# Kernel optimization log

Measured on AMD Instinct MI355X. Metric: run time of the kernel, lower is better.

The kernel has to match this reference:

```python
import jax, jax.numpy as jnp
import numpy as np

B, T, D = 128, 1024, 1024


def setup_inputs() -> dict:
    key = jax.random.key(0)
    ks = jax.random.split(key, 6)
    s = 0.02  # small init scale for weights
    return {
        "z_eeg": jax.random.normal(ks[0], (B, T, D), dtype=jnp.float32),
        "z_rppg": jax.random.normal(ks[1], (B, D), dtype=jnp.float32),
        "Wq": jax.random.normal(ks[2], (D, D), dtype=jnp.float32) * s,
        "Wk": jax.random.normal(ks[3], (D, D), dtype=jnp.float32) * s,
        "Wm_w": jax.random.normal(ks[4], (D, D), dtype=jnp.float32) * s,
        "Wm_b": jnp.zeros((D,), dtype=jnp.float32),
        "Wf_w": jax.random.normal(ks[5], (2 * D, D), dtype=jnp.float32) * s,
        "Wf_b": jnp.zeros((D,), dtype=jnp.float32),
        "bf": jnp.zeros((D,), dtype=jnp.float32),
    }


def reference(z_eeg, z_rppg, Wq, Wk, Wm_w, Wm_b, Wf_w, Wf_b, bf):
    d = Wq.shape[-1]
    Q = z_rppg @ Wq                                    # [B, D]
    K = jnp.einsum("btd,de->bte", z_eeg, Wk)          # [B, T, D]
    scores = jnp.einsum("bd,btd->bt", Q, K) / jnp.sqrt(jnp.float32(d))  # [B, T]
    w = jax.nn.softmax(scores, axis=1)                 # [B, T]
    A = jnp.einsum("bt,btd->bd", w, z_eeg)            # attention-pooled EEG [B, D]
    concat = jnp.concatenate([A, z_rppg], axis=-1)     # [B, 2D]
    f = jax.nn.sigmoid(concat @ Wf_w + Wf_b + bf)      # gate [B, D]
    m = A @ Wm_w + Wm_b                                # [B, D]
    h = jax.nn.relu(z_rppg + m * f)                    # gated residual fusion
    return h
```

## Files before the change

kernel.cpp:

```cpp
#include <hip/hip_runtime.h>
#include <hip/hip_bf16.h>


#define BB   128
#define TT   1024
#define DD   1024
#define NT   16
#define KS   32
#define QS   4

__global__ __launch_bounds__(256) void k_gemm_ab(const float* __restrict__ X,
                                                 const float* __restrict__ W,
                                                 float* __restrict__ Cpart) {
  const int t = threadIdx.x;
  const int ebase = blockIdx.x * 64;
  const int bbase = blockIdx.y * 16;
  const int p = blockIdx.z;
  const int e = ebase + (t & 63);
  const int bg = t >> 6;
  __shared__ __align__(16) float Xs[16][64];
  float acc[4] = {0.f, 0.f, 0.f, 0.f};
  const int kend = p * 256 + 256;
  for (int k0 = p * 256; k0 < kend; k0 += 64) {
#pragma unroll
    for (int j = 0; j < 4; ++j) {
      int i = t + 256 * j;
      Xs[i >> 6][i & 63] = X[(size_t)(bbase + (i >> 6)) * DD + k0 + (i & 63)];
    }
    __syncthreads();
#pragma unroll 16
    for (int kk = 0; kk < 64; ++kk) {
      float w = W[(size_t)(k0 + kk) * DD + e];
#pragma unroll
      for (int j = 0; j < 4; ++j) acc[j] = fmaf(Xs[bg + 4 * j][kk], w, acc[j]);
    }
    __syncthreads();
  }
#pragma unroll
  for (int j = 0; j < 4; ++j)
    Cpart[(size_t)p * BB * DD + (size_t)(bbase + bg + 4 * j) * DD + e] = acc[j];
}

__global__ __launch_bounds__(256) void k_gemm_abt(const float* __restrict__ Qpart,
                                                  const float* __restrict__ W,
                                                  float* __restrict__ Cpart) {
  const int t = threadIdx.x;
  const int dbase = blockIdx.x * 64;
  const int bbase = blockIdx.y * 16;
  const int p = blockIdx.z;
  const int dl = t & 63;
  const int bg = t >> 6;
  __shared__ __align__(16) float Xs[16][64];
  __shared__ __align__(16) float Ws[64][65];
  float acc[4] = {0.f, 0.f, 0.f, 0.f};
  const int kend = p * 256 + 256;
  for (int k0 = p * 256; k0 < kend; k0 += 64) {
#pragma unroll
    for (int j = 0; j < 4; ++j) {
      int i = t + 256 * j;
      const size_t base = (size_t)(bbase + (i >> 6)) * DD + k0 + (i & 63);
      float v = Qpart[base] + Qpart[base + (size_t)BB * DD] +
                Qpart[base + 2 * (size_t)BB * DD] + Qpart[base + 3 * (size_t)BB * DD];
      Xs[i >> 6][i & 63] = v;
    }
#pragma unroll
    for (int j = 0; j < 16; ++j) {
      int i = t + 256 * j;
      Ws[i >> 6][i & 63] = W[(size_t)(dbase + (i >> 6)) * DD + k0 + (i & 63)];
    }
    __syncthreads();
#pragma unroll 8
    for (int kk = 0; kk < 64; ++kk) {
      float w = Ws[dl][kk];
#pragma unroll
      for (int j = 0; j < 4; ++j) acc[j] = fmaf(Xs[bg + 4 * j][kk], w, acc[j]);
    }
    __syncthreads();
  }
#pragma unroll
  for (int j = 0; j < 4; ++j)
    Cpart[(size_t)p * BB * DD + (size_t)(bbase + bg + 4 * j) * DD + dbase + dl] = acc[j];
}

__global__ __launch_bounds__(256) void k_attn(const float* __restrict__ z_eeg,
                                              const float* __restrict__ Qkpart,
                                              float* __restrict__ Npart,
                                              float* __restrict__ Zpart) {
  const int t = threadIdx.x;
  const int lane = t & 63;
  const int w = t >> 6;
  const int tblk = blockIdx.x;
  const int b = blockIdx.y;

  float4 qk4[4];
#pragma unroll
  for (int q = 0; q < 4; ++q) {
    float4 a = ((const float4*)(Qkpart + (size_t)b * DD))[q * 64 + lane];
#pragma unroll
    for (int pp = 1; pp < QS; ++pp) {
      float4 s = ((const float4*)(Qkpart + ((size_t)pp * BB + b) * DD))[q * 64 + lane];
      a.x += s.x; a.y += s.y; a.z += s.z; a.w += s.w;
    }
    a.x *= 0.03125f; a.y *= 0.03125f; a.z *= 0.03125f; a.w *= 0.03125f;
    qk4[q] = a;
  }

  float4 acc[4] = {};
  float zsum = 0.f;
  const float4* zb = (const float4*)(z_eeg + (size_t)b * TT * DD);
  const int row0 = tblk * 64 + w;

  float4 cA[4], cB[4];
  {
    const float4* pA = zb + (size_t)row0 * 256;
    const float4* pB = zb + (size_t)(row0 + 4) * 256;
#pragma unroll
    for (int q = 0; q < 4; ++q) cA[q] = pA[q * 64 + lane];
#pragma unroll
    for (int q = 0; q < 4; ++q) cB[q] = pB[q * 64 + lane];
  }
#pragma unroll
  for (int i = 0; i < 8; ++i) {
    float4 nA[4], nB[4];
    if (i < 7) {
      const float4* pA = zb + (size_t)(row0 + (i + 1) * 8) * 256;
      const float4* pB = zb + (size_t)(row0 + (i + 1) * 8 + 4) * 256;
#pragma unroll
      for (int q = 0; q < 4; ++q) nA[q] = pA[q * 64 + lane];
#pragma unroll
      for (int q = 0; q < 4; ++q) nB[q] = pB[q * 64 + lane];
    }
    float dotA = 0.f, dotB = 0.f;
#pragma unroll
    for (int q = 0; q < 4; ++q) {
      dotA += cA[q].x * qk4[q].x + cA[q].y * qk4[q].y + cA[q].z * qk4[q].z + cA[q].w * qk4[q].w;
      dotB += cB[q].x * qk4[q].x + cB[q].y * qk4[q].y + cB[q].z * qk4[q].z + cB[q].w * qk4[q].w;
    }
#pragma unroll
    for (int off = 32; off >= 1; off >>= 1) {
      dotA += __shfl_xor(dotA, off);
      dotB += __shfl_xor(dotB, off);
    }
    const float eA = __expf(dotA);
    const float eB = __expf(dotB);
    zsum += eA + eB;
#pragma unroll
    for (int q = 0; q < 4; ++q) {
      acc[q].x = fmaf(eA, cA[q].x, acc[q].x);
      acc[q].y = fmaf(eA, cA[q].y, acc[q].y);
      acc[q].z = fmaf(eA, cA[q].z, acc[q].z);
      acc[q].w = fmaf(eA, cA[q].w, acc[q].w);
      acc[q].x = fmaf(eB, cB[q].x, acc[q].x);
      acc[q].y = fmaf(eB, cB[q].y, acc[q].y);
      acc[q].z = fmaf(eB, cB[q].z, acc[q].z);
      acc[q].w = fmaf(eB, cB[q].w, acc[q].w);
    }
    if (i < 7) {
#pragma unroll
      for (int q = 0; q < 4; ++q) { cA[q] = nA[q]; cB[q] = nB[q]; }
    }
  }

  __shared__ __align__(16) float4 sacc[3][256];
  __shared__ float szw[4];
  if (w > 0) {
#pragma unroll
    for (int q = 0; q < 4; ++q) sacc[w - 1][q * 64 + lane] = acc[q];
  }
  if (lane == 0) szw[w] = zsum;
  __syncthreads();
  if (w == 0) {
    float4* np = (float4*)(Npart + ((size_t)b * NT + tblk) * DD);
#pragma unroll
    for (int q = 0; q < 4; ++q) {
      float4 a = acc[q];
#pragma unroll
      for (int ww = 0; ww < 3; ++ww) {
        float4 s = sacc[ww][q * 64 + lane];
        a.x += s.x; a.y += s.y; a.z += s.z; a.w += s.w;
      }
      np[q * 64 + lane] = a;
    }
    if (lane == 0) Zpart[b * NT + tblk] = szw[0] + szw[1] + szw[2] + szw[3];
  }
}

__global__ __launch_bounds__(256) void k_reduce_a(const float* __restrict__ Npart,
                                                  const float* __restrict__ Zpart,
                                                  float* __restrict__ A) {
  const int idx = blockIdx.x * 256 + threadIdx.x;
  const int b = idx >> 10;
  const int d = idx & 1023;
  float n = 0.f, z = 0.f;
#pragma unroll
  for (int k = 0; k < NT; ++k) {
    n += Npart[((size_t)b * NT + k) * DD + d];
    z += Zpart[b * NT + k];
  }
  A[idx] = n / z;
}

__device__ __forceinline__ void outer_acc(float4 acc[4], const float4 a, const float4 w) {
  acc[0].x = fmaf(a.x, w.x, acc[0].x); acc[0].y = fmaf(a.x, w.y, acc[0].y);
  acc[0].z = fmaf(a.x, w.z, acc[0].z); acc[0].w = fmaf(a.x, w.w, acc[0].w);
  acc[1].x = fmaf(a.y, w.x, acc[1].x); acc[1].y = fmaf(a.y, w.y, acc[1].y);
  acc[1].z = fmaf(a.y, w.z, acc[1].z); acc[1].w = fmaf(a.y, w.w, acc[1].w);
  acc[2].x = fmaf(a.z, w.x, acc[2].x); acc[2].y = fmaf(a.z, w.y, acc[2].y);
  acc[2].z = fmaf(a.z, w.z, acc[2].z); acc[2].w = fmaf(a.z, w.w, acc[2].w);
  acc[3].x = fmaf(a.w, w.x, acc[3].x); acc[3].y = fmaf(a.w, w.y, acc[3].y);
  acc[3].z = fmaf(a.w, w.z, acc[3].z); acc[3].w = fmaf(a.w, w.w, acc[3].w);
}

__global__ __launch_bounds__(256) void k_epi_partial(const float* __restrict__ A,
                                                     const float* __restrict__ z_rppg,
                                                     const float* __restrict__ Wf_w,
                                                     const float* __restrict__ Wm_w,
                                                     float* __restrict__ fpart,
                                                     float* __restrict__ mpart) {
  const int t = threadIdx.x;
  const int dbase = blockIdx.x * 32;
  const int ks = blockIdx.y;
  const int bq = t >> 3;
  const int dg = t & 7;
  __shared__ __align__(16) float Cst[32][132];
  __shared__ __align__(16) float Ws[32][36];
  float4 accf[4] = {};
  float4 accm[4] = {};

  {
    const float* src = (ks < 16) ? (A + ks * 64) : (z_rppg + ks * 64 - 1024);
    const float* wsrc = Wf_w + (size_t)ks * 64 * DD;
    for (int k0 = 0; k0 < 64; k0 += 32) {
#pragma unroll
      for (int j = 0; j < 16; ++j) {
        int i = t + 256 * j; int bb = i >> 5, c = i & 31;
        Cst[c][bb] = src[(size_t)bb * DD + k0 + c];
      }
#pragma unroll
      for (int j = 0; j < 4; ++j) {
        int i = t + 256 * j; int r = i >> 5, c = i & 31;
        Ws[r][c] = wsrc[(size_t)(k0 + r) * DD + dbase + c];
      }
      __syncthreads();
#pragma unroll
      for (int kk = 0; kk < 32; ++kk) {
        float4 a4 = *(const float4*)&Cst[kk][bq * 4];
        float4 w4 = *(const float4*)&Ws[kk][dg * 4];
        outer_acc(accf, a4, w4);
      }
      __syncthreads();
    }
  }
  {
    const float* src = A + ks * 32;
    const float* wsrc = Wm_w + (size_t)ks * 32 * DD;
#pragma unroll
    for (int j = 0; j < 16; ++j) {
      int i = t + 256 * j; int bb = i >> 5, c = i & 31;
      Cst[c][bb] = src[(size_t)bb * DD + c];
    }
#pragma unroll
    for (int j = 0; j < 4; ++j) {
      int i = t + 256 * j; int r = i >> 5, c = i & 31;
      Ws[r][c] = wsrc[(size_t)r * DD + dbase + c];
    }
    __syncthreads();
#pragma unroll
    for (int kk = 0; kk < 32; ++kk) {
      float4 a4 = *(const float4*)&Cst[kk][bq * 4];
      float4 w4 = *(const float4*)&Ws[kk][dg * 4];
      outer_acc(accm, a4, w4);
    }
  }
#pragma unroll
  for (int i = 0; i < 4; ++i) {
    const int b = bq * 4 + i;
    *(float4*)&fpart[(size_t)ks * (BB * DD) + (size_t)b * DD + dbase + dg * 4] = accf[i];
    *(float4*)&mpart[(size_t)ks * (BB * DD) + (size_t)b * DD + dbase + dg * 4] = accm[i];
  }
}

__global__ __launch_bounds__(256) void k_combine(const float* __restrict__ fpart,
                                                 const float* __restrict__ mpart,
                                                 const float* __restrict__ Wf_b,
                                                 const float* __restrict__ bf,
                                                 const float* __restrict__ Wm_b,
                                                 const float* __restrict__ z_rppg,
                                                 float* __restrict__ out) {
  const int idx = blockIdx.x * 256 + threadIdx.x;
  const int d = idx & 1023;
  float f = Wf_b[d] + bf[d];
  float m = Wm_b[d];
#pragma unroll
  for (int k = 0; k < KS; ++k) {
    f += fpart[(size_t)k * (BB * DD) + idx];
    m += mpart[(size_t)k * (BB * DD) + idx];
  }
  const float g = 1.f / (1.f + __expf(-f));
  const float h = z_rppg[idx] + m * g;
  out[idx] = h > 0.f ? h : 0.f;
}

extern "C" void kernel_launch(void* const* d_in, const int* in_sizes, int n_in,
                              void* d_out, int out_size, void* d_ws, size_t ws_size,
                              hipStream_t stream) {
  const float* z_eeg  = (const float*)d_in[0];
  const float* z_rppg = (const float*)d_in[1];
  const float* Wq     = (const float*)d_in[2];
  const float* Wk     = (const float*)d_in[3];
  const float* Wm_w   = (const float*)d_in[4];
  const float* Wm_b   = (const float*)d_in[5];
  const float* Wf_w   = (const float*)d_in[6];
  const float* Wf_b   = (const float*)d_in[7];
  const float* bf     = (const float*)d_in[8];
  float* out = (float*)d_out;

  float* ws = (float*)d_ws;
  float* Qpart  = ws;
  float* Qkpart = Qpart + (size_t)QS * BB * DD;
  float* Npart  = Qkpart + (size_t)QS * BB * DD;
  float* Zpart  = Npart + (size_t)BB * NT * DD;
  float* A      = Zpart + BB * NT;
  float* fpart  = A + (size_t)BB * DD;
  float* mpart  = fpart + (size_t)KS * BB * DD;

  k_gemm_ab<<<dim3(16, 8, QS), 256, 0, stream>>>(z_rppg, Wq, Qpart);
  k_gemm_abt<<<dim3(16, 8, QS), 256, 0, stream>>>(Qpart, Wk, Qkpart);
  k_attn<<<dim3(NT, BB), 256, 0, stream>>>(z_eeg, Qkpart, Npart, Zpart);
  k_reduce_a<<<(BB * DD) / 256, 256, 0, stream>>>(Npart, Zpart, A);
  k_epi_partial<<<dim3(32, KS), 256, 0, stream>>>(A, z_rppg, Wf_w, Wm_w, fpart, mpart);
  k_combine<<<(BB * DD) / 256, 256, 0, stream>>>(fpart, mpart, Wf_b, bf, Wm_b, z_rppg, out);
}
```

Before: 225.9 us.

## Fuse all stages into one persistent kernel with software grid barriers

Replaces six separate kernel launches with a single persistent kernel of 256 blocks that runs the Q GEMM, Wk projection, attention pooling, normalization, gate/mix GEMMs and combine in sequence. Stages are separated by atomic-counter grid barriers. Work partitioning changes: attention uses two blocks per batch row, and the epilogue uses 16 K-splits instead of 32. This aims to remove launch gaps and shrink partial-sum buffers. The tradeoffs are low occupancy during the bandwidth-heavy attention pass and a reliance on all blocks being co-resident.

Measured after the change: 260.1 us. +15.2%, slower.

```diff
diff --git a/kernel.cpp b/kernel.cpp
--- a/kernel.cpp
+++ b/kernel.cpp
@@ -5,199 +5,32 @@
 #define BB   128
 #define TT   1024
 #define DD   1024
-#define NT   16
-#define KS   32
+#define NB   256
+#define NTH  512
 #define QS   4
-
-__global__ __launch_bounds__(256) void k_gemm_ab(const float* __restrict__ X,
-                                                 const float* __restrict__ W,
-                                                 float* __restrict__ Cpart) {
-  const int t = threadIdx.x;
-  const int ebase = blockIdx.x * 64;
-  const int bbase = blockIdx.y * 16;
-  const int p = blockIdx.z;
-  const int e = ebase + (t & 63);
-  const int bg = t >> 6;
-  __shared__ __align__(16) float Xs[16][64];
-  float acc[4] = {0.f, 0.f, 0.f, 0.f};
-  const int kend = p * 256 + 256;
-  for (int k0 = p * 256; k0 < kend; k0 += 64) {
-#pragma unroll
-    for (int j = 0; j < 4; ++j) {
-      int i = t + 256 * j;
-      Xs[i >> 6][i & 63] = X[(size_t)(bbase + (i >> 6)) * DD + k0 + (i & 63)];
-    }
-    __syncthreads();
-#pragma unroll 16
-    for (int kk = 0; kk < 64; ++kk) {
-      float w = W[(size_t)(k0 + kk) * DD + e];
-#pragma unroll
-      for (int j = 0; j < 4; ++j) acc[j] = fmaf(Xs[bg + 4 * j][kk], w, acc[j]);
-    }
-    __syncthreads();
-  }
-#pragma unroll
-  for (int j = 0; j < 4; ++j)
-    Cpart[(size_t)p * BB * DD + (size_t)(bbase + bg + 4 * j) * DD + e] = acc[j];
-}
-
-__global__ __launch_bounds__(256) void k_gemm_abt(const float* __restrict__ Qpart,
-                                                  const float* __restrict__ W,
-                                                  float* __restrict__ Cpart) {
-  const int t = threadIdx.x;
-  const int dbase = blockIdx.x * 64;
-  const int bbase = blockIdx.y * 16;
-  const int p = blockIdx.z;
-  const int dl = t & 63;
-  const int bg = t >> 6;
-  __shared__ __align__(16) float Xs[16][64];
-  __shared__ __align__(16) float Ws[64][65];
-  float acc[4] = {0.f, 0.f, 0.f, 0.f};
-  const int kend = p * 256 + 256;
-  for (int k0 = p * 256; k0 < kend; k0 += 64) {
-#pragma unroll
-    for (int j = 0; j < 4; ++j) {
-      int i = t + 256 * j;
-      const size_t base = (size_t)(bbase + (i >> 6)) * DD + k0 + (i & 63);
-      float v = Qpart[base] + Qpart[base + (size_t)BB * DD] +
-                Qpart[base + 2 * (size_t)BB * DD] + Qpart[base + 3 * (size_t)BB * DD];
-      Xs[i >> 6][i & 63] = v;
-    }
-#pragma unroll
-    for (int j = 0; j < 16; ++j) {
-      int i = t + 256 * j;
-      Ws[i >> 6][i & 63] = W[(size_t)(dbase + (i >> 6)) * DD + k0 + (i & 63)];
-    }
-    __syncthreads();
-#pragma unroll 8
-    for (int kk = 0; kk < 64; ++kk) {
-      float w = Ws[dl][kk];
-#pragma unroll
-      for (int j = 0; j < 4; ++j) acc[j] = fmaf(Xs[bg + 4 * j][kk], w, acc[j]);
-    }
-    __syncthreads();
-  }
-#pragma unroll
-  for (int j = 0; j < 4; ++j)
-    Cpart[(size_t)p * BB * DD + (size_t)(bbase + bg + 4 * j) * DD + dbase + dl] = acc[j];
-}
-
-__global__ __launch_bounds__(256) void k_attn(const float* __restrict__ z_eeg,
-                                              const float* __restrict__ Qkpart,
-                                              float* __restrict__ Npart,
-                                              float* __restrict__ Zpart) {
-  const int t = threadIdx.x;
-  const int lane = t & 63;
-  const int w = t >> 6;
-  const int tblk = blockIdx.x;
-  const int b = blockIdx.y;
-
-  float4 qk4[4];
-#pragma unroll
-  for (int q = 0; q < 4; ++q) {
-    float4 a = ((const float4*)(Qkpart + (size_t)b * DD))[q * 64 + lane];
-#pragma unroll
-    for (int pp = 1; pp < QS; ++pp) {
-      float4 s = ((const float4*)(Qkpart + ((size_t)pp * BB + b) * DD))[q * 64 + lane];
-      a.x += s.x; a.y += s.y; a.z += s.z; a.w += s.w;
-    }
-    a.x *= 0.03125f; a.y *= 0.03125f; a.z *= 0.03125f; a.w *= 0.03125f;
-    qk4[q] = a;
-  }
-
-  float4 acc[4] = {};
-  float zsum = 0.f;
-  const float4* zb = (const float4*)(z_eeg + (size_t)b * TT * DD);
-  const int row0 = tblk * 64 + w;
-
-  float4 cA[4], cB[4];
-  {
-    const float4* pA = zb + (size_t)row0 * 256;
-    const float4* pB = zb + (size_t)(row0 + 4) * 256;
-#pragma unroll
-    for (int q = 0; q < 4; ++q) cA[q] = pA[q * 64 + lane];
-#pragma unroll
-    for (int q = 0; q < 4; ++q) cB[q] = pB[q * 64 + lane];
-  }
-#pragma unroll
-  for (int i = 0; i < 8; ++i) {
-    float4 nA[4], nB[4];
-    if (i < 7) {
-      const float4* pA = zb + (size_t)(row0 + (i + 1) * 8) * 256;
-      const float4* pB = zb + (size_t)(row0 + (i + 1) * 8 + 4) * 256;
-#pragma unroll
-      for (int q = 0; q < 4; ++q) nA[q] = pA[q * 64 + lane];
-#pragma unroll
-      for (int q = 0; q < 4; ++q) nB[q] = pB[q * 64 + lane];
-    }
-    float dotA = 0.f, dotB = 0.f;
-#pragma unroll
-    for (int q = 0; q < 4; ++q) {
-      dotA += cA[q].x * qk4[q].x + cA[q].y * qk4[q].y + cA[q].z * qk4[q].z + cA[q].w * qk4[q].w;
-      dotB += cB[q].x * qk4[q].x + cB[q].y * qk4[q].y + cB[q].z * qk4[q].z + cB[q].w * qk4[q].w;
-    }
-#pragma unroll
-    for (int off = 32; off >= 1; off >>= 1) {
-      dotA += __shfl_xor(dotA, off);
-      dotB += __shfl_xor(dotB, off);
-    }
-    const float eA = __expf(dotA);
-    const float eB = __expf(dotB);
-    zsum += eA + eB;
-#pragma unroll
-    for (int q = 0; q < 4; ++q) {
-      acc[q].x = fmaf(eA, cA[q].x, acc[q].x);
-      acc[q].y = fmaf(eA, cA[q].y, acc[q].y);
-      acc[q].z = fmaf(eA, cA[q].z, acc[q].z);
-      acc[q].w = fmaf(eA, cA[q].w, acc[q].w);
-      acc[q].x = fmaf(eB, cB[q].x, acc[q].x);
-      acc[q].y = fmaf(eB, cB[q].y, acc[q].y);
-      acc[q].z = fmaf(eB, cB[q].z, acc[q].z);
-      acc[q].w = fmaf(eB, cB[q].w, acc[q].w);
-    }
-    if (i < 7) {
-#pragma unroll
-      for (int q = 0; q < 4; ++q) { cA[q] = nA[q]; cB[q] = nB[q]; }
-    }
-  }
-
-  __shared__ __align__(16) float4 sacc[3][256];
-  __shared__ float szw[4];
-  if (w > 0) {
-#pragma unroll
-    for (int q = 0; q < 4; ++q) sacc[w - 1][q * 64 + lane] = acc[q];
-  }
-  if (lane == 0) szw[w] = zsum;
+#define KSE  16
+
+union SharedU {
+  struct { float Xs[16][64]; float Ws[128][65]; } g;
+  struct { float4 sacc[8][256]; float szw[8]; } a;
+  struct { float Cst[32][132]; float Wst[32][68]; } e;
+};
+
+__device__ __forceinline__ void gsync(int* cnt, int* rel, int gen) {
   __syncthreads();
-  if (w == 0) {
-    float4* np = (float4*)(Npart + ((size_t)b * NT + tblk) * DD);
-#pragma unroll
-    for (int q = 0; q < 4; ++q) {
-      float4 a = acc[q];
-#pragma unroll
-      for (int ww = 0; ww < 3; ++ww) {
-        float4 s = sacc[ww][q * 64 + lane];
-        a.x += s.x; a.y += s.y; a.z += s.z; a.w += s.w;
-      }
-      np[q * 64 + lane] = a;
-    }
-    if (lane == 0) Zpart[b * NT + tblk] = szw[0] + szw[1] + szw[2] + szw[3];
-  }
-}
-
-__global__ __launch_bounds__(256) void k_reduce_a(const float* __restrict__ Npart,
-                                                  const float* __restrict__ Zpart,
-                                                  float* __restrict__ A) {
-  const int idx = blockIdx.x * 256 + threadIdx.x;
-  const int b = idx >> 10;
-  const int d = idx & 1023;
-  float n = 0.f, z = 0.f;
-#pragma unroll
-  for (int k = 0; k < NT; ++k) {
-    n += Npart[((size_t)b * NT + k) * DD + d];
-    z += Zpart[b * NT + k];
-  }
-  A[idx] = n / z;
+  if (threadIdx.x == 0) {
+    __threadfence();
+    int old = __hip_atomic_fetch_add(cnt, 1, __ATOMIC_RELAXED, __HIP_MEMORY_SCOPE_AGENT);
+    if (old == NB * gen - 1) {
+      __hip_atomic_store(rel, gen, __ATOMIC_RELAXED, __HIP_MEMORY_SCOPE_AGENT);
+    } else {
+      while (__hip_atomic_load(rel, __ATOMIC_RELAXED, __HIP_MEMORY_SCOPE_AGENT) < gen) {
+        __builtin_amdgcn_s_sleep(2);
+      }
+    }
+    __threadfence();
+  }
+  __syncthreads();
 }
 
 __device__ __forceinline__ void outer_acc(float4 acc[4], const float4 a, const float4 w) {
@@ -211,94 +44,268 @@
   acc[3].z = fmaf(a.w, w.z, acc[3].z); acc[3].w = fmaf(a.w, w.w, acc[3].w);
 }
 
-__global__ __launch_bounds__(256) void k_epi_partial(const float* __restrict__ A,
-                                                     const float* __restrict__ z_rppg,
-                                                     const float* __restrict__ Wf_w,
-                                                     const float* __restrict__ Wm_w,
-                                                     float* __restrict__ fpart,
-                                                     float* __restrict__ mpart) {
+__global__ __launch_bounds__(NTH, 2) void k_fused(
+    const float* __restrict__ z_eeg, const float* __restrict__ z_rppg,
+    const float* __restrict__ Wq, const float* __restrict__ Wk,
+    const float* __restrict__ Wm_w, const float* __restrict__ Wm_b,
+    const float* __restrict__ Wf_w, const float* __restrict__ Wf_b,
+    const float* __restrict__ bfp, float* __restrict__ out,
+    float* __restrict__ Qpart, float* __restrict__ Qkpart,
+    float* __restrict__ Npart, float* __restrict__ Zpart,
+    float* __restrict__ A, float* __restrict__ fpart, float* __restrict__ mpart,
+    int* cnt, int* rel) {
+  __shared__ SharedU sh;
   const int t = threadIdx.x;
-  const int dbase = blockIdx.x * 32;
-  const int ks = blockIdx.y;
-  const int bq = t >> 3;
-  const int dg = t & 7;
-  __shared__ __align__(16) float Cst[32][132];
-  __shared__ __align__(16) float Ws[32][36];
-  float4 accf[4] = {};
-  float4 accm[4] = {};
-
-  {
-    const float* src = (ks < 16) ? (A + ks * 64) : (z_rppg + ks * 64 - 1024);
-    const float* wsrc = Wf_w + (size_t)ks * 64 * DD;
-    for (int k0 = 0; k0 < 64; k0 += 32) {
+  const int bid = blockIdx.x;
+
+  {
+    const int ebase = (bid & 7) * 128;
+    const int bbase = ((bid >> 3) & 7) * 16;
+    const int p = bid >> 6;
+    const int e = ebase + (t & 127);
+    const int bg = t >> 7;
+    float acc[4] = {0.f, 0.f, 0.f, 0.f};
+    const int kend = p * 256 + 256;
+    for (int k0 = p * 256; k0 < kend; k0 += 64) {
+#pragma unroll
+      for (int j = 0; j < 2; ++j) {
+        int i = t + NTH * j;
+        sh.g.Xs[i >> 6][i & 63] = z_rppg[(size_t)(bbase + (i >> 6)) * DD + k0 + (i & 63)];
+      }
+      __syncthreads();
+#pragma unroll 16
+      for (int kk = 0; kk < 64; ++kk) {
+        float w = Wq[(size_t)(k0 + kk) * DD + e];
+#pragma unroll
+        for (int j = 0; j < 4; ++j) acc[j] = fmaf(sh.g.Xs[bg + 4 * j][kk], w, acc[j]);
+      }
+      __syncthreads();
+    }
+#pragma unroll
+    for (int j = 0; j < 4; ++j)
+      Qpart[(size_t)p * BB * DD + (size_t)(bbase + bg + 4 * j) * DD + e] = acc[j];
+  }
+  gsync(cnt, rel, 1);
+
+  {
+    const int dbase = (bid & 7) * 128;
+    const int bbase = ((bid >> 3) & 7) * 16;
+    const int p = bid >> 6;
+    const int dl = t & 127;
+    const int bg = t >> 7;
+    float acc[4] = {0.f, 0.f, 0.f, 0.f};
+    const int kend = p * 256 + 256;
+    for (int k0 = p * 256; k0 < kend; k0 += 64) {
+#pragma unroll
+      for (int j = 0; j < 2; ++j) {
+        int i = t + NTH * j;
+        const size_t base = (size_t)(bbase + (i >> 6)) * DD + k0 + (i & 63);
+        sh.g.Xs[i >> 6][i & 63] = Qpart[base] + Qpart[base + (size_t)BB * DD] +
+                                  Qpart[base + 2 * (size_t)BB * DD] +
+                                  Qpart[base + 3 * (size_t)BB * DD];
+      }
 #pragma unroll
       for (int j = 0; j < 16; ++j) {
-        int i = t + 256 * j; int bb = i >> 5, c = i & 31;
-        Cst[c][bb] = src[(size_t)bb * DD + k0 + c];
-      }
-#pragma unroll
-      for (int j = 0; j < 4; ++j) {
-        int i = t + 256 * j; int r = i >> 5, c = i & 31;
-        Ws[r][c] = wsrc[(size_t)(k0 + r) * DD + dbase + c];
+        int i = t + NTH * j;
+        sh.g.Ws[i >> 6][i & 63] = Wk[(size_t)(dbase + (i >> 6)) * DD + k0 + (i & 63)];
       }
       __syncthreads();
-#pragma unroll
-      for (int kk = 0; kk < 32; ++kk) {
-        float4 a4 = *(const float4*)&Cst[kk][bq * 4];
-        float4 w4 = *(const float4*)&Ws[kk][dg * 4];
-        outer_acc(accf, a4, w4);
+#pragma unroll 8
+      for (int kk = 0; kk < 64; ++kk) {
+        float w = sh.g.Ws[dl][kk];
+#pragma unroll
+        for (int j = 0; j < 4; ++j) acc[j] = fmaf(sh.g.Xs[bg + 4 * j][kk], w, acc[j]);
       }
       __syncthreads();
     }
-  }
-  {
-    const float* src = A + ks * 32;
-    const float* wsrc = Wm_w + (size_t)ks * 32 * DD;
-#pragma unroll
-    for (int j = 0; j < 16; ++j) {
-      int i = t + 256 * j; int bb = i >> 5, c = i & 31;
-      Cst[c][bb] = src[(size_t)bb * DD + c];
-    }
-#pragma unroll
-    for (int j = 0; j < 4; ++j) {
-      int i = t + 256 * j; int r = i >> 5, c = i & 31;
-      Ws[r][c] = wsrc[(size_t)r * DD + dbase + c];
-    }
+#pragma unroll
+    for (int j = 0; j < 4; ++j)
+      Qkpart[(size_t)p * BB * DD + (size_t)(bbase + bg + 4 * j) * DD + dbase + dl] = acc[j];
+  }
+  gsync(cnt, rel, 2);
+
+  {
+    const int b = bid >> 1;
+    const int th = bid & 1;
+    const int lane = t & 63;
+    const int w = t >> 6;
+
+    float4 qk4[4];
+#pragma unroll
+    for (int q = 0; q < 4; ++q) {
+      float4 a = ((const float4*)(Qkpart + (size_t)b * DD))[q * 64 + lane];
+#pragma unroll
+      for (int pp = 1; pp < QS; ++pp) {
+        float4 s = ((const float4*)(Qkpart + ((size_t)pp * BB + b) * DD))[q * 64 + lane];
+        a.x += s.x; a.y += s.y; a.z += s.z; a.w += s.w;
+      }
+      a.x *= 0.03125f; a.y *= 0.03125f; a.z *= 0.03125f; a.w *= 0.03125f;
+      qk4[q] = a;
+    }
+
+    float4 acc[4] = {};
+    float zsum = 0.f;
+    const float4* zb = (const float4*)(z_eeg + (size_t)b * TT * DD);
+    const int rbase = th * 512 + w * 4;
+
+    for (int i = 0; i < 16; ++i) {
+      const int r0 = rbase + i * 32;
+      const float4* p0 = zb + (size_t)(r0 + 0) * 256;
+      const float4* p1 = zb + (size_t)(r0 + 1) * 256;
+      const float4* p2 = zb + (size_t)(r0 + 2) * 256;
+      const float4* p3 = zb + (size_t)(r0 + 3) * 256;
+      float4 z0[4], z1[4], z2[4], z3[4];
+#pragma unroll
+      for (int q = 0; q < 4; ++q) z0[q] = p0[q * 64 + lane];
+#pragma unroll
+      for (int q = 0; q < 4; ++q) z1[q] = p1[q * 64 + lane];
+#pragma unroll
+      for (int q = 0; q < 4; ++q) z2[q] = p2[q * 64 + lane];
+#pragma unroll
+      for (int q = 0; q < 4; ++q) z3[q] = p3[q * 64 + lane];
+      float d0 = 0.f, d1 = 0.f, d2 = 0.f, d3 = 0.f;
+#pragma unroll
+      for (int q = 0; q < 4; ++q) {
+        d0 += z0[q].x * qk4[q].x + z0[q].y * qk4[q].y + z0[q].z * qk4[q].z + z0[q].w * qk4[q].w;
+        d1 += z1[q].x * qk4[q].x + z1[q].y * qk4[q].y + z1[q].z * qk4[q].z + z1[q].w * qk4[q].w;
+        d2 += z2[q].x * qk4[q].x + z2[q].y * qk4[q].y + z2[q].z * qk4[q].z + z2[q].w * qk4[q].w;
+        d3 += z3[q].x * qk4[q].x + z3[q].y * qk4[q].y + z3[q].z * qk4[q].z + z3[q].w * qk4[q].w;
+      }
+#pragma unroll
+      for (int off = 32; off >= 1; off >>= 1) {
+        d0 += __shfl_xor(d0, off);
+        d1 += __shfl_xor(d1, off);
+        d2 += __shfl_xor(d2, off);
+        d3 += __shfl_xor(d3, off);
+      }
+      const float e0 = __expf(d0);
+      const float e1 = __expf(d1);
+      const float e2 = __expf(d2);
+      const float e3 = __expf(d3);
+      zsum += e0 + e1 + e2 + e3;
+#pragma unroll
+      for (int q = 0; q < 4; ++q) {
+        acc[q].x = fmaf(e0, z0[q].x, acc[q].x); acc[q].y = fmaf(e0, z0[q].y, acc[q].y);
+        acc[q].z = fmaf(e0, z0[q].z, acc[q].z); acc[q].w = fmaf(e0, z0[q].w, acc[q].w);
+        acc[q].x = fmaf(e1, z1[q].x, acc[q].x); acc[q].y = fmaf(e1, z1[q].y, acc[q].y);
+        acc[q].z = fmaf(e1, z1[q].z, acc[q].z); acc[q].w = fmaf(e1, z1[q].w, acc[q].w);
+        acc[q].x = fmaf(e2, z2[q].x, acc[q].x); acc[q].y = fmaf(e2, z2[q].y, acc[q].y);
+        acc[q].z = fmaf(e2, z2[q].z, acc[q].z); acc[q].w = fmaf(e2, z2[q].w, acc[q].w);
+        acc[q].x = fmaf(e3, z3[q].x, acc[q].x); acc[q].y = fmaf(e3, z3[q].y, acc[q].y);
+        acc[q].z = fmaf(e3, z3[q].z, acc[q].z); acc[q].w = fmaf(e3, z3[q].w, acc[q].w);
+      }
+    }
+
+#pragma unroll
+    for (int q = 0; q < 4; ++q) sh.a.sacc[w][q * 64 + lane] = acc[q];
+    if (lane == 0) sh.a.szw[w] = zsum;
     __syncthreads();
-#pragma unroll
-    for (int kk = 0; kk < 32; ++kk) {
-      float4 a4 = *(const float4*)&Cst[kk][bq * 4];
-      float4 w4 = *(const float4*)&Ws[kk][dg * 4];
-      outer_acc(accm, a4, w4);
-    }
-  }
-#pragma unroll
-  for (int i = 0; i < 4; ++i) {
-    const int b = bq * 4 + i;
-    *(float4*)&fpart[(size_t)ks * (BB * DD) + (size_t)b * DD + dbase + dg * 4] = accf[i];
-    *(float4*)&mpart[(size_t)ks * (BB * DD) + (size_t)b * DD + dbase + dg * 4] = accm[i];
-  }
-}
-
-__global__ __launch_bounds__(256) void k_combine(const float* __restrict__ fpart,
-                                                 const float* __restrict__ mpart,
-                                                 const float* __restrict__ Wf_b,
-                                                 const float* __restrict__ bf,
-                                                 const float* __restrict__ Wm_b,
-                                                 const float* __restrict__ z_rppg,
-                                                 float* __restrict__ out) {
-  const int idx = blockIdx.x * 256 + threadIdx.x;
-  const int d = idx & 1023;
-  float f = Wf_b[d] + bf[d];
-  float m = Wm_b[d];
-#pragma unroll
-  for (int k = 0; k < KS; ++k) {
-    f += fpart[(size_t)k * (BB * DD) + idx];
-    m += mpart[(size_t)k * (BB * DD) + idx];
-  }
-  const float g = 1.f / (1.f + __expf(-f));
-  const float h = z_rppg[idx] + m * g;
-  out[idx] = h > 0.f ? h : 0.f;
+    if (t < 256) {
+      float4 s = sh.a.sacc[0][t];
+#pragma unroll
+      for (int ww = 1; ww < 8; ++ww) {
+        float4 v = sh.a.sacc[ww][t];
+        s.x += v.x; s.y += v.y; s.z += v.z; s.w += v.w;
+      }
+      ((float4*)(Npart + (size_t)bid * DD))[t] = s;
+      if (t == 0) {
+        float z = 0.f;
+#pragma unroll
+        for (int ww = 0; ww < 8; ++ww) z += sh.a.szw[ww];
+        Zpart[bid] = z;
+      }
+    }
+  }
+  gsync(cnt, rel, 3);
+
+  {
+    const int idx = bid * NTH + t;
+    const int b = idx >> 10;
+    const int d = idx & 1023;
+    float n = Npart[(size_t)(2 * b) * DD + d] + Npart[(size_t)(2 * b + 1) * DD + d];
+    float z = Zpart[2 * b] + Zpart[2 * b + 1];
+    A[idx] = n / z;
+  }
+  gsync(cnt, rel, 4);
+
+  {
+    const int dbase = (bid & 15) * 64;
+    const int ks = bid >> 4;
+    const int bq = t >> 4;
+    const int dg = t & 15;
+    float4 accf[4] = {};
+    float4 accm[4] = {};
+    {
+      const float* src = (ks < 8) ? (A + ks * 128) : (z_rppg + (ks - 8) * 128);
+      const float* wsrc = Wf_w + (size_t)ks * 128 * DD;
+      for (int k0 = 0; k0 < 128; k0 += 32) {
+#pragma unroll
+        for (int j = 0; j < 8; ++j) {
+          int i = t + NTH * j; int bb = i >> 5, c = i & 31;
+          sh.e.Cst[c][bb] = src[(size_t)bb * DD + k0 + c];
+        }
+#pragma unroll
+        for (int j = 0; j < 4; ++j) {
+          int i = t + NTH * j; int r = i >> 6, c = i & 63;
+          sh.e.Wst[r][c] = wsrc[(size_t)(k0 + r) * DD + dbase + c];
+        }
+        __syncthreads();
+#pragma unroll
+        for (int kk = 0; kk < 32; ++kk) {
+          float4 a4 = *(const float4*)&sh.e.Cst[kk][bq * 4];
+          float4 w4 = *(const float4*)&sh.e.Wst[kk][dg * 4];
+          outer_acc(accf, a4, w4);
+        }
+        __syncthreads();
+      }
+    }
+    {
+      const float* src = A + ks * 64;
+      const float* wsrc = Wm_w + (size_t)ks * 64 * DD;
+      for (int k0 = 0; k0 < 64; k0 += 32) {
+#pragma unroll
+        for (int j = 0; j < 8; ++j) {
+          int i = t + NTH * j; int bb = i >> 5, c = i & 31;
+          sh.e.Cst[c][bb] = src[(size_t)bb * DD + k0 + c];
+        }
+#pragma unroll
+        for (int j = 0; j < 4; ++j) {
+          int i = t + NTH * j; int r = i >> 6, c = i & 63;
+          sh.e.Wst[r][c] = wsrc[(size_t)(k0 + r) * DD + dbase + c];
+        }
+        __syncthreads();
+#pragma unroll
+        for (int kk = 0; kk < 32; ++kk) {
+          float4 a4 = *(const float4*)&sh.e.Cst[kk][bq * 4];
+          float4 w4 = *(const float4*)&sh.e.Wst[kk][dg * 4];
+          outer_acc(accm, a4, w4);
+        }
+        __syncthreads();
+      }
+    }
+#pragma unroll
+    for (int i = 0; i < 4; ++i) {
+      const int b = bq * 4 + i;
+      *(float4*)&fpart[(size_t)ks * (BB * DD) + (size_t)b * DD + dbase + dg * 4] = accf[i];
+      *(float4*)&mpart[(size_t)ks * (BB * DD) + (size_t)b * DD + dbase + dg * 4] = accm[i];
+    }
+  }
+  gsync(cnt, rel, 5);
+
+  {
+    const int idx = bid * NTH + t;
+    const int d = idx & 1023;
+    float f = Wf_b[d] + bfp[d];
+    float m = Wm_b[d];
+#pragma unroll
+    for (int k = 0; k < KSE; ++k) {
+      f += fpart[(size_t)k * (BB * DD) + idx];
+      m += mpart[(size_t)k * (BB * DD) + idx];
+    }
+    const float g = 1.f / (1.f + __expf(-f));
+    const float h = z_rppg[idx] + m * g;
+    out[idx] = h > 0.f ? h : 0.f;
+  }
 }
 
 extern "C" void kernel_launch(void* const* d_in, const int* in_sizes, int n_in,
@@ -312,22 +319,23 @@
   const float* Wm_b   = (const float*)d_in[5];
   const float* Wf_w   = (const float*)d_in[6];
   const float* Wf_b   = (const float*)d_in[7];
-  const float* bf     = (const float*)d_in[8];
+  const float* bfp    = (const float*)d_in[8];
   float* out = (float*)d_out;
 
-  float* ws = (float*)d_ws;
-  float* Qpart  = ws;
+  int* cnt = (int*)d_ws;
+  int* rel = cnt + 1;
+  hipMemsetAsync(d_ws, 0, 16, stream);
+
+  float* base   = (float*)d_ws + 256;
+  float* Qpart  = base;
   float* Qkpart = Qpart + (size_t)QS * BB * DD;
   float* Npart  = Qkpart + (size_t)QS * BB * DD;
-  float* Zpart  = Npart + (size_t)BB * NT * DD;
-  float* A      = Zpart + BB * NT;
+  float* Zpart  = Npart + (size_t)2 * BB * DD;
+  float* A      = Zpart + 2 * BB;
   float* fpart  = A + (size_t)BB * DD;
-  float* mpart  = fpart + (size_t)KS * BB * DD;
-
-  k_gemm_ab<<<dim3(16, 8, QS), 256, 0, stream>>>(z_rppg, Wq, Qpart);
-  k_gemm_abt<<<dim3(16, 8, QS), 256, 0, stream>>>(Qpart, Wk, Qkpart);
-  k_attn<<<dim3(NT, BB), 256, 0, stream>>>(z_eeg, Qkpart, Npart, Zpart);
-  k_reduce_a<<<(BB * DD) / 256, 256, 0, stream>>>(Npart, Zpart, A);
-  k_epi_partial<<<dim3(32, KS), 256, 0, stream>>>(A, z_rppg, Wf_w, Wm_w, fpart, mpart);
-  k_combine<<<(BB * DD) / 256, 256, 0, stream>>>(fpart, mpart, Wf_b, bf, Wm_b, z_rppg, out);
+  float* mpart  = fpart + (size_t)KSE * BB * DD;
+
+  k_fused<<<NB, NTH, 0, stream>>>(z_eeg, z_rppg, Wq, Wk, Wm_w, Wm_b, Wf_w, Wf_b,
+                                  bfp, out, Qpart, Qkpart, Npart, Zpart, A,
+                                  fpart, mpart, cnt, rel);
 }
```
